# Kernel optimization log

Hardware: AMD Instinct MI355X
Metric: run time of the kernel (lower is better)

Reference implementation:

```python
import jax, jax.numpy as jnp
import numpy as np

BATCH = 8192
EMBED_DIM = 256
INPUT_DIM = 3 * EMBED_DIM  # 768
NUM_LAYERS = 4
VOCAB_SIZES = [100000, 100000, 1000]
EPS = 1e-5


def setup_inputs() -> dict:
    key = jax.random.key(0)
    ks = jax.random.split(key, 20)
    inp = {}
    inp["x_p"] = jax.random.randint(ks[0], (BATCH,), 0, VOCAB_SIZES[0])
    inp["x_a"] = jax.random.randint(ks[1], (BATCH,), 0, VOCAB_SIZES[1])
    inp["x_c"] = jax.random.randint(ks[2], (BATCH,), 0, VOCAB_SIZES[2])
    inp["y_true"] = jax.random.uniform(ks[3], (BATCH, 1), dtype=jnp.float32)
    # embedding tables (nn.Embedding default init N(0,1))
    inp["E0"] = jax.random.normal(ks[4], (VOCAB_SIZES[0], EMBED_DIM), dtype=jnp.float32)
    inp["E1"] = jax.random.normal(ks[5], (VOCAB_SIZES[1], EMBED_DIM), dtype=jnp.float32)
    inp["E2"] = jax.random.normal(ks[6], (VOCAB_SIZES[2], EMBED_DIM), dtype=jnp.float32)
    lim = 1.0 / np.sqrt(INPUT_DIM)
    inp["Wd"] = jax.random.uniform(ks[7], (NUM_LAYERS, INPUT_DIM, INPUT_DIM), jnp.float32, -lim, lim)
    inp["bd"] = jnp.zeros((NUM_LAYERS, INPUT_DIM), jnp.float32)
    inp["Ws"] = jax.random.uniform(ks[8], (NUM_LAYERS, INPUT_DIM, INPUT_DIM), jnp.float32, -lim, lim)
    inp["bs"] = jnp.zeros((NUM_LAYERS, INPUT_DIM), jnp.float32)
    inp["wfd"] = jax.random.uniform(ks[9], (INPUT_DIM,), jnp.float32, -lim, lim)
    inp["bfd"] = jax.random.uniform(ks[10], (), jnp.float32, -lim, lim)
    inp["wfs"] = jax.random.uniform(ks[11], (INPUT_DIM,), jnp.float32, -lim, lim)
    inp["bfs"] = jax.random.uniform(ks[12], (), jnp.float32, -lim, lim)
    return inp


def _cross_network(x, W, b, net_id, mask_key):
    # per layer: cross = x @ W[l].T + b[l]; mask = bernoulli(sigmoid(layernorm over FULL tensor)); x += cross*mask
    for l in range(NUM_LAYERS):
        cross = jnp.einsum("bd,od->bo", x, W[l]) + b[l]
        m = jnp.mean(cross)
        v = jnp.mean(jnp.square(cross - m))  # F.layer_norm(x, x.size()): normalize over all elements
        ln = (cross - m) * jax.lax.rsqrt(v + EPS)
        p = jax.nn.sigmoid(ln)
        k = jax.random.fold_in(mask_key, net_id * NUM_LAYERS + l)
        mask = jax.random.bernoulli(k, p).astype(x.dtype)
        x = x + cross * mask
    return x


def _bce(p, y):
    return jnp.mean(-(y * jnp.log(p) + (1.0 - y) * jnp.log(1.0 - p)))


def reference(x_p, x_a, x_c, y_true, E0, E1, E2, Wd, bd, Ws, bs, wfd, bfd, wfs, bfs):
    h = EMBED_DIM // 2
    e0, e1, e2 = E0[x_p], E1[x_a], E2[x_c]  # [B, embed_dim] each
    e_a = jnp.concatenate([e0[:, :h], e1[:, :h], e2[:, :h]], axis=-1)
    e_b = jnp.concatenate([e0[:, h:], e1[:, h:], e2[:, h:]], axis=-1)
    x = jnp.concatenate([e_a, e_b], axis=-1)  # [B, 3*embed_dim]

    mask_key = jax.random.key(42)
    x_d = _cross_network(x, Wd, bd, 0, mask_key)
    x_s = _cross_network(x, Ws, bs, 1, mask_key)

    sd_d = jax.nn.sigmoid(x_d @ wfd + bfd)[:, None]  # fc_d(x_d)
    ss_s = jax.nn.sigmoid(x_s @ wfs + bfs)[:, None]  # fc_s(x_s)
    sd_s = jax.nn.sigmoid(x_s @ wfd + bfd)[:, None]  # fc_d(x_s)
    ss_d = jax.nn.sigmoid(x_d @ wfs + bfs)[:, None]  # fc_s(x_d)
    y_pred_d = 0.5 * (sd_d + ss_s)
    y_pred_s = 0.5 * (sd_s + ss_d)

    loss_d = _bce(y_pred_d, y_true)
    loss_s = _bce(y_pred_s, y_true)
    bce_loss = loss_d + loss_s
    weight_d = jnp.maximum(0.0, loss_d - bce_loss)
    weight_s = jnp.maximum(0.0, loss_s - bce_loss)
    tri_loss = bce_loss + weight_d * loss_d + weight_s * loss_s
    return (y_pred_d, tri_loss)
```

## Files before the change

### kernel.cpp

```cpp
#include <hip/hip_runtime.h>
#include <hip/hip_bf16.h>
#include <cstdint>
#include <cstddef>

#define BATCH   8192
#define DIM     768
#define NTOT    6291456
#define NLAYERS 4

typedef _Float16 half8 __attribute__((ext_vector_type(8)));
typedef float    f32x4 __attribute__((ext_vector_type(4)));

#define AS_GLOBAL __attribute__((address_space(1)))
#define AS_LDS    __attribute__((address_space(3)))

__device__ __forceinline__ void async_copy16(const void* g, void* l) {
  __builtin_amdgcn_global_load_lds((AS_GLOBAL const uint32_t*)g,
                                   (AS_LDS uint32_t*)l, 16, 0, 0);
}

__host__ __device__ __forceinline__ uint32_t rotl32(uint32_t v, int d) {
  return (v << d) | (v >> (32 - d));
}

__host__ __device__ __forceinline__ void threefry2x32(
    uint32_t k0, uint32_t k1, uint32_t x0, uint32_t x1,
    uint32_t& o0, uint32_t& o1) {
  uint32_t ks2 = k0 ^ k1 ^ 0x1BD11BDAu;
  x0 += k0; x1 += k1;
#define TF_R(r) { x0 += x1; x1 = rotl32(x1, (r)) ^ x0; }
  TF_R(13) TF_R(15) TF_R(26) TF_R(6)
  x0 += k1; x1 += ks2 + 1u;
  TF_R(17) TF_R(29) TF_R(16) TF_R(24)
  x0 += ks2; x1 += k0 + 2u;
  TF_R(13) TF_R(15) TF_R(26) TF_R(6)
  x0 += k0; x1 += k1 + 3u;
  TF_R(17) TF_R(29) TF_R(16) TF_R(24)
  x0 += k1; x1 += ks2 + 4u;
  TF_R(13) TF_R(15) TF_R(26) TF_R(6)
  x0 += ks2; x1 += k0 + 5u;
#undef TF_R
  o0 = x0; o1 = x1;
}

__device__ __forceinline__ double sigmoid_d(double x) {
  return 1.0 / (1.0 + exp(-x));
}

__global__ __launch_bounds__(256) void gather_kernel(
    const int* __restrict__ x_p, const int* __restrict__ x_a,
    const int* __restrict__ x_c,
    const float* __restrict__ E0, const float* __restrict__ E1,
    const float* __restrict__ E2,
    _Float16* __restrict__ xdh, _Float16* __restrict__ xdl,
    _Float16* __restrict__ xsh, _Float16* __restrict__ xsl) {
  int j = blockIdx.x * 256 + threadIdx.x;
  int b = j / DIM;
  int f = j - b * DIM;
  int half_ = f / 384;
  int w = f - half_ * 384;
  int t = w >> 7;
  int c = (w & 127) + (half_ << 7);
  int idx;
  const float* E;
  if (t == 0)      { E = E0; idx = x_p[b]; }
  else if (t == 1) { E = E1; idx = x_a[b]; }
  else             { E = E2; idx = x_c[b]; }
  float v = E[(size_t)idx * 256 + c];
  _Float16 h = (_Float16)v;
  _Float16 l = (_Float16)(v - (float)h);
  xdh[j] = h; xdl[j] = l;
  xsh[j] = h; xsl[j] = l;
}

__global__ __launch_bounds__(256) void split_w_kernel(
    const float* __restrict__ Wd, const float* __restrict__ Ws,
    _Float16* __restrict__ Wh, _Float16* __restrict__ Wl) {
  int idx = blockIdx.x * 256 + threadIdx.x;
  const int perNet = NLAYERS * DIM * DIM;
  float v = (idx < perNet) ? Wd[idx] : Ws[idx - perNet];
  _Float16 h = (_Float16)v;
  Wh[idx] = h;
  Wl[idx] = (_Float16)(v - (float)h);
}

__global__ __launch_bounds__(256, 3) void gemm_mfma_kernel(
    const _Float16* __restrict__ xdh, const _Float16* __restrict__ xdl,
    const _Float16* __restrict__ xsh, const _Float16* __restrict__ xsl,
    const _Float16* __restrict__ Wh, const _Float16* __restrict__ Wl,
    const float* __restrict__ bd, const float* __restrict__ bs,
    float* __restrict__ crd, float* __restrict__ crs,
    double* __restrict__ partials, int layer) {
  const int net = blockIdx.z;
  const float* bias = (net ? bs : bd) + layer * DIM;
  float* C = net ? crs : crd;

  const int wave = threadIdx.x >> 6, lane = threadIdx.x & 63;
  const int quad = lane >> 4, l16 = lane & 15;
  const int m0 = blockIdx.x * 128;
  const int n0 = blockIdx.y * 128;

  __shared__ _Float16 lds[4 * 5120];

  const _Float16* gbase;
  int rowbase;
  switch (wave) {
    case 0:  gbase = net ? xsh : xdh; rowbase = m0; break;
    case 1:  gbase = net ? xsl : xdl; rowbase = m0; break;
    case 2:  gbase = Wh + ((size_t)net * NLAYERS + layer) * DIM * DIM; rowbase = n0; break;
    default: gbase = Wl + ((size_t)net * NLAYERS + layer) * DIM * DIM; rowbase = n0; break;
  }
  int soff[10];
#pragma unroll
  for (int j = 0; j < 10; ++j) {
    int s  = j * 64 + lane;
    int r  = (s * 52429) >> 18;
    int kk = (s - 5 * r) & 3;
    soff[j] = (rowbase + r) * DIM + kk * 8;
  }
  _Float16* ldsw = &lds[wave * 5120];

  const int wm = (wave >> 1) * 64, wn = (wave & 1) * 64;
  const int fslotA = ((wm + l16) * 5 + quad) * 8;
  const int fslotB = ((wn + l16) * 5 + quad) * 8;

  f32x4 acc[4][4];
#pragma unroll
  for (int i = 0; i < 4; ++i)
#pragma unroll
    for (int j = 0; j < 4; ++j) acc[i][j] = (f32x4){0.f, 0.f, 0.f, 0.f};

  for (int k0 = 0; k0 < DIM; k0 += 32) {
    __syncthreads();
#pragma unroll
    for (int j = 0; j < 10; ++j)
      async_copy16(gbase + soff[j] + k0, ldsw + j * 512);
    __syncthreads();

    half8 ah[4], al[4], bh[4], bl[4];
#pragma unroll
    for (int t = 0; t < 4; ++t) {
      ah[t] = *(const half8*)&lds[        fslotA + t * 640];
      al[t] = *(const half8*)&lds[ 5120 + fslotA + t * 640];
      bh[t] = *(const half8*)&lds[10240 + fslotB + t * 640];
      bl[t] = *(const half8*)&lds[15360 + fslotB + t * 640];
    }
#pragma unroll
    for (int mt = 0; mt < 4; ++mt)
#pragma unroll
      for (int nt = 0; nt < 4; ++nt) {
        f32x4 a = acc[mt][nt];
        a = __builtin_amdgcn_mfma_f32_16x16x32_f16(ah[mt], bh[nt], a, 0, 0, 0);
        a = __builtin_amdgcn_mfma_f32_16x16x32_f16(al[mt], bh[nt], a, 0, 0, 0);
        a = __builtin_amdgcn_mfma_f32_16x16x32_f16(ah[mt], bl[nt], a, 0, 0, 0);
        acc[mt][nt] = a;
      }
  }

  float biasv[4];
#pragma unroll
  for (int nt = 0; nt < 4; ++nt) biasv[nt] = bias[n0 + wn + nt * 16 + l16];

  double s = 0.0, q = 0.0;
#pragma unroll
  for (int mt = 0; mt < 4; ++mt) {
#pragma unroll
    for (int nt = 0; nt < 4; ++nt) {
      int n = n0 + wn + nt * 16 + l16;
#pragma unroll
      for (int r = 0; r < 4; ++r) {
        int m = m0 + wm + mt * 16 + quad * 4 + r;
        float v = acc[mt][nt][r] + biasv[nt];
        C[(size_t)m * DIM + n] = v;
        s += (double)v;
        q += (double)v * (double)v;
      }
    }
  }
#pragma unroll
  for (int off = 32; off > 0; off >>= 1) {
    s += __shfl_down(s, off);
    q += __shfl_down(q, off);
  }
  __shared__ double red[4][2];
  if (lane == 0) { red[wave][0] = s; red[wave][1] = q; }
  __syncthreads();
  if (threadIdx.x == 0) {
    double S = red[0][0] + red[1][0] + red[2][0] + red[3][0];
    double Q = red[0][1] + red[1][1] + red[2][1] + red[3][1];
    int bid = blockIdx.y * 64 + blockIdx.x;
    partials[((size_t)net * 384 + bid) * 2 + 0] = S;
    partials[((size_t)net * 384 + bid) * 2 + 1] = Q;
  }
}

__global__ __launch_bounds__(256) void finalize_stats_kernel(
    const double* __restrict__ partials, double* __restrict__ stats) {
  int net = blockIdx.x;
  const double* P = partials + (size_t)net * 384 * 2;
  int tid = threadIdx.x;
  double s = 0.0, q = 0.0;
  for (int i = tid; i < 384; i += 256) {
    s += P[i * 2 + 0];
    q += P[i * 2 + 1];
  }
#pragma unroll
  for (int off = 32; off > 0; off >>= 1) {
    s += __shfl_down(s, off);
    q += __shfl_down(q, off);
  }
  __shared__ double red[4][2];
  int wave = tid >> 6, lane = tid & 63;
  if (lane == 0) { red[wave][0] = s; red[wave][1] = q; }
  __syncthreads();
  if (tid == 0) {
    stats[net * 2 + 0] = red[0][0] + red[1][0] + red[2][0] + red[3][0];
    stats[net * 2 + 1] = red[0][1] + red[1][1] + red[2][1] + red[3][1];
  }
}

__global__ __launch_bounds__(256) void mask_update_kernel(
    _Float16* __restrict__ xdh, _Float16* __restrict__ xdl,
    _Float16* __restrict__ xsh, _Float16* __restrict__ xsl,
    const float* __restrict__ crd, const float* __restrict__ crs,
    const double* __restrict__ stats,
    uint32_t kd0, uint32_t kd1, uint32_t ks0, uint32_t ks1) {
  const int net = blockIdx.y;
  _Float16* xh = net ? xsh : xdh;
  _Float16* xl = net ? xsl : xdl;
  const float* cr = net ? crs : crd;
  const uint32_t k0 = net ? ks0 : kd0;
  const uint32_t k1 = net ? ks1 : kd1;

  const double invN = 1.0 / (double)NTOT;
  double meand = stats[net * 2 + 0] * invN;
  double vard  = stats[net * 2 + 1] * invN - meand * meand;
  float m  = (float)meand;
  float v  = (float)vard;
  float sv = v + 1e-5f;
  float rs = (float)(1.0 / sqrt((double)sv));

  uint32_t j = blockIdx.x * 256u + threadIdx.x;
  float c = cr[j];
  float ln = (c - m) * rs;
  float p = (float)sigmoid_d((double)ln);
  uint32_t o0, o1;
  threefry2x32(k0, k1, 0u, j, o0, o1);
  uint32_t bits = o0 ^ o1;
  float u = __uint_as_float(0x3F800000u | (bits >> 9)) - 1.0f;

  float xv = (float)xh[j] + (float)xl[j];
  if (u < p) xv += c;
  _Float16 h = (_Float16)xv;
  xh[j] = h;
  xl[j] = (_Float16)(xv - (float)h);
}

__global__ __launch_bounds__(256) void head_kernel(
    const _Float16* __restrict__ xdh, const _Float16* __restrict__ xdl,
    const _Float16* __restrict__ xsh, const _Float16* __restrict__ xsl,
    const float* __restrict__ wfd, const float* __restrict__ wfs,
    const float* __restrict__ bfd_p, const float* __restrict__ bfs_p,
    const float* __restrict__ y_true,
    float* __restrict__ out, double* __restrict__ bce_part) {
  const int wave = threadIdx.x >> 6;
  const int lane = threadIdx.x & 63;
  const int row = blockIdx.x * 4 + wave;
  const size_t base = (size_t)row * DIM;

  float dd = 0.f, dsw = 0.f, sd = 0.f, ssw = 0.f;
  for (int t = lane; t < DIM; t += 64) {
    float vd = (float)xdh[base + t] + (float)xdl[base + t];
    float vs = (float)xsh[base + t] + (float)xsl[base + t];
    float wd = wfd[t], ws = wfs[t];
    dd  = fmaf(vd, wd, dd);
    dsw = fmaf(vd, ws, dsw);
    sd  = fmaf(vs, wd, sd);
    ssw = fmaf(vs, ws, ssw);
  }
#pragma unroll
  for (int off = 32; off > 0; off >>= 1) {
    dd  += __shfl_down(dd, off);
    dsw += __shfl_down(dsw, off);
    sd  += __shfl_down(sd, off);
    ssw += __shfl_down(ssw, off);
  }
  __shared__ double redd[4], reds[4];
  if (lane == 0) {
    float bfd = *bfd_p, bfs = *bfs_p;
    double sdd = sigmoid_d((double)(dd + bfd));
    double ssd = sigmoid_d((double)(dsw + bfs));
    double sds = sigmoid_d((double)(sd + bfd));
    double sss = sigmoid_d((double)(ssw + bfs));
    double ypd = 0.5 * (sdd + sss);
    double yps = 0.5 * (sds + ssd);
    out[row] = (float)ypd;
    double y = (double)y_true[row];
    redd[wave] = -(y * log(ypd) + (1.0 - y) * log(1.0 - ypd));
    reds[wave] = -(y * log(yps) + (1.0 - y) * log(1.0 - yps));
  }
  __syncthreads();
  if (threadIdx.x == 0) {
    bce_part[(size_t)blockIdx.x * 2 + 0] = redd[0] + redd[1] + redd[2] + redd[3];
    bce_part[(size_t)blockIdx.x * 2 + 1] = reds[0] + reds[1] + reds[2] + reds[3];
  }
}

__global__ __launch_bounds__(256) void loss_kernel(
    const double* __restrict__ bce_part, float* __restrict__ out_tri) {
  int tid = threadIdx.x;
  double sdl = 0.0, ssl = 0.0;
  for (int i = tid; i < 2048; i += 256) {
    sdl += bce_part[i * 2 + 0];
    ssl += bce_part[i * 2 + 1];
  }
#pragma unroll
  for (int off = 32; off > 0; off >>= 1) {
    sdl += __shfl_down(sdl, off);
    ssl += __shfl_down(ssl, off);
  }
  __shared__ double red[4][2];
  int wave = tid >> 6, lane = tid & 63;
  if (lane == 0) { red[wave][0] = sdl; red[wave][1] = ssl; }
  __syncthreads();
  if (tid == 0) {
    double loss_d = (red[0][0] + red[1][0] + red[2][0] + red[3][0]) / (double)BATCH;
    double loss_s = (red[0][1] + red[1][1] + red[2][1] + red[3][1]) / (double)BATCH;
    double bce = loss_d + loss_s;
    double wd = fmax(0.0, loss_d - bce);
    double ws = fmax(0.0, loss_s - bce);
    out_tri[0] = (float)(bce + wd * loss_d + ws * loss_s);
  }
}

extern "C" void kernel_launch(void* const* d_in, const int* in_sizes, int n_in,
                              void* d_out, int out_size, void* d_ws, size_t ws_size,
                              hipStream_t stream) {
  const int* x_p = (const int*)d_in[0];
  const int* x_a = (const int*)d_in[1];
  const int* x_c = (const int*)d_in[2];
  const float* y_true = (const float*)d_in[3];
  const float* E0 = (const float*)d_in[4];
  const float* E1 = (const float*)d_in[5];
  const float* E2 = (const float*)d_in[6];
  const float* Wd = (const float*)d_in[7];
  const float* bd = (const float*)d_in[8];
  const float* Ws = (const float*)d_in[9];
  const float* bs = (const float*)d_in[10];
  const float* wfd = (const float*)d_in[11];
  const float* bfd = (const float*)d_in[12];
  const float* wfs = (const float*)d_in[13];
  const float* bfs = (const float*)d_in[14];
  float* out = (float*)d_out;

  char* p = (char*)d_ws;
  float* crd = (float*)p;                 p += (size_t)NTOT * 4;
  float* crs = (float*)p;                 p += (size_t)NTOT * 4;
  double* partials = (double*)p;          p += (size_t)2 * 384 * 2 * 8;
  double* stats    = (double*)p;          p += 4 * 8;
  double* bce_part = (double*)p;          p += (size_t)2048 * 2 * 8;
  _Float16* xdh = (_Float16*)p;           p += (size_t)NTOT * 2;
  _Float16* xdl = (_Float16*)p;           p += (size_t)NTOT * 2;
  _Float16* xsh = (_Float16*)p;           p += (size_t)NTOT * 2;
  _Float16* xsl = (_Float16*)p;           p += (size_t)NTOT * 2;
  _Float16* Wh  = (_Float16*)p;           p += (size_t)2 * NLAYERS * DIM * DIM * 2;
  _Float16* Wl  = (_Float16*)p;           p += (size_t)2 * NLAYERS * DIM * DIM * 2;

  gather_kernel<<<NTOT / 256, 256, 0, stream>>>(
      x_p, x_a, x_c, E0, E1, E2, xdh, xdl, xsh, xsl);
  split_w_kernel<<<2 * NLAYERS * DIM * DIM / 256, 256, 0, stream>>>(Wd, Ws, Wh, Wl);

  for (int l = 0; l < NLAYERS; ++l) {
    gemm_mfma_kernel<<<dim3(64, 6, 2), 256, 0, stream>>>(
        xdh, xdl, xsh, xsl, Wh, Wl, bd, bs, crd, crs, partials, l);
    finalize_stats_kernel<<<2, 256, 0, stream>>>(partials, stats);
    uint32_t kd0, kd1, ks0, ks1;
    threefry2x32(0u, 42u, 0u, (uint32_t)l, kd0, kd1);
    threefry2x32(0u, 42u, 0u, (uint32_t)(4 + l), ks0, ks1);
    mask_update_kernel<<<dim3(NTOT / 256, 2), 256, 0, stream>>>(
        xdh, xdl, xsh, xsl, crd, crs, stats, kd0, kd1, ks0, ks1);
  }

  head_kernel<<<BATCH / 4, 256, 0, stream>>>(
      xdh, xdl, xsh, xsl, wfd, wfs, bfd, bfs, y_true, out, bce_part);
  loss_kernel<<<1, 256, 0, stream>>>(bce_part, out + BATCH);
}
```

Baseline: 800.6 us.

## Retile GEMM with double-buffered LDS, atomic stats, and vectorized elementwise kernels

```diff
diff --git a/kernel.cpp b/kernel.cpp
--- a/kernel.cpp
+++ b/kernel.cpp
@@ -9,6 +9,7 @@
 #define NLAYERS 4
 
 typedef _Float16 half8 __attribute__((ext_vector_type(8)));
+typedef _Float16 half4 __attribute__((ext_vector_type(4)));
 typedef float    f32x4 __attribute__((ext_vector_type(4)));
 
 #define AS_GLOBAL __attribute__((address_space(1)))
@@ -47,30 +48,63 @@
   return 1.0 / (1.0 + exp(-x));
 }
 
+__device__ __forceinline__ double dexp(double x) {
+  x = fmin(fmax(x, -708.0), 708.0);
+  const double LOG2E = 1.4426950408889634;
+  const double LN2   = 0.6931471805599453;
+  double t = x * LOG2E;
+  double n = rint(t);
+  double g = (t - n) * LN2;
+  double r = 2.7557319223985893e-07;
+  r = r * g + 2.7557319223985888e-06;
+  r = r * g + 2.4801587301587302e-05;
+  r = r * g + 1.9841269841269841e-04;
+  r = r * g + 1.3888888888888889e-03;
+  r = r * g + 8.3333333333333332e-03;
+  r = r * g + 4.1666666666666664e-02;
+  r = r * g + 1.6666666666666666e-01;
+  r = r * g + 0.5;
+  r = r * g + 1.0;
+  r = r * g + 1.0;
+  int ni = (int)n;
+  double sc = __longlong_as_double(((long long)(1023 + ni)) << 52);
+  return r * sc;
+}
+
 __global__ __launch_bounds__(256) void gather_kernel(
     const int* __restrict__ x_p, const int* __restrict__ x_a,
     const int* __restrict__ x_c,
     const float* __restrict__ E0, const float* __restrict__ E1,
     const float* __restrict__ E2,
     _Float16* __restrict__ xdh, _Float16* __restrict__ xdl,
-    _Float16* __restrict__ xsh, _Float16* __restrict__ xsl) {
-  int j = blockIdx.x * 256 + threadIdx.x;
-  int b = j / DIM;
-  int f = j - b * DIM;
+    _Float16* __restrict__ xsh, _Float16* __restrict__ xsl,
+    double* __restrict__ stats, double* __restrict__ bce_acc) {
+  if (blockIdx.x == 0 && threadIdx.x < 18) {
+    if (threadIdx.x < 16) stats[threadIdx.x] = 0.0;
+    else bce_acc[threadIdx.x - 16] = 0.0;
+  }
+  int j4  = blockIdx.x * 256 + threadIdx.x;
+  int idx = j4 * 4;
+  int b = idx / DIM;
+  int f = idx - b * DIM;
   int half_ = f / 384;
   int w = f - half_ * 384;
   int t = w >> 7;
   int c = (w & 127) + (half_ << 7);
-  int idx;
+  int row;
   const float* E;
-  if (t == 0)      { E = E0; idx = x_p[b]; }
-  else if (t == 1) { E = E1; idx = x_a[b]; }
-  else             { E = E2; idx = x_c[b]; }
-  float v = E[(size_t)idx * 256 + c];
-  _Float16 h = (_Float16)v;
-  _Float16 l = (_Float16)(v - (float)h);
-  xdh[j] = h; xdl[j] = l;
-  xsh[j] = h; xsl[j] = l;
+  if (t == 0)      { E = E0; row = x_p[b]; }
+  else if (t == 1) { E = E1; row = x_a[b]; }
+  else             { E = E2; row = x_c[b]; }
+  f32x4 v = *(const f32x4*)&E[(size_t)row * 256 + c];
+  half4 h, l;
+#pragma unroll
+  for (int i = 0; i < 4; ++i) {
+    h[i] = (_Float16)v[i];
+    l[i] = (_Float16)(v[i] - (float)h[i]);
+  }
+  *(half4*)&xdh[idx] = h; *(half4*)&xdl[idx] = l;
+  *(half4*)&xsh[idx] = h; *(half4*)&xsl[idx] = l;
 }
 
 __global__ __launch_bounds__(256) void split_w_kernel(
@@ -84,138 +118,127 @@
   Wl[idx] = (_Float16)(v - (float)h);
 }
 
-__global__ __launch_bounds__(256, 3) void gemm_mfma_kernel(
+__global__ __launch_bounds__(512, 2) void gemm_mfma_kernel(
     const _Float16* __restrict__ xdh, const _Float16* __restrict__ xdl,
     const _Float16* __restrict__ xsh, const _Float16* __restrict__ xsl,
     const _Float16* __restrict__ Wh, const _Float16* __restrict__ Wl,
     const float* __restrict__ bd, const float* __restrict__ bs,
     float* __restrict__ crd, float* __restrict__ crs,
-    double* __restrict__ partials, int layer) {
+    double* __restrict__ stats, int layer) {
   const int net = blockIdx.z;
   const float* bias = (net ? bs : bd) + layer * DIM;
   float* C = net ? crs : crd;
 
-  const int wave = threadIdx.x >> 6, lane = threadIdx.x & 63;
+  const int tid  = threadIdx.x;
+  const int wave = tid >> 6, lane = tid & 63;
   const int quad = lane >> 4, l16 = lane & 15;
   const int m0 = blockIdx.x * 128;
-  const int n0 = blockIdx.y * 128;
-
-  __shared__ _Float16 lds[4 * 5120];
+  const int n0 = blockIdx.y * 384;
+
+  __shared__ _Float16 lds[2][32768];
+  __shared__ double red[8][2];
 
   const _Float16* gbase;
-  int rowbase;
-  switch (wave) {
-    case 0:  gbase = net ? xsh : xdh; rowbase = m0; break;
-    case 1:  gbase = net ? xsl : xdl; rowbase = m0; break;
-    case 2:  gbase = Wh + ((size_t)net * NLAYERS + layer) * DIM * DIM; rowbase = n0; break;
-    default: gbase = Wl + ((size_t)net * NLAYERS + layer) * DIM * DIM; rowbase = n0; break;
-  }
-  int soff[10];
-#pragma unroll
-  for (int j = 0; j < 10; ++j) {
-    int s  = j * 64 + lane;
-    int r  = (s * 52429) >> 18;
-    int kk = (s - 5 * r) & 3;
+  int chunkoff, rows, rowbase;
+  if (wave == 0)      { gbase = net ? xsh : xdh; chunkoff = 0; rows = 128; rowbase = m0; }
+  else if (wave == 1) { gbase = net ? xsl : xdl; chunkoff = 0; rows = 128; rowbase = m0; }
+  else if (wave < 5)  { gbase = Wh + ((size_t)net * NLAYERS + layer) * DIM * DIM;
+                        chunkoff = (wave - 2) * 512; rows = 384; rowbase = n0; }
+  else                { gbase = Wl + ((size_t)net * NLAYERS + layer) * DIM * DIM;
+                        chunkoff = (wave - 5) * 512; rows = 384; rowbase = n0; }
+  int soff[8];
+#pragma unroll
+  for (int j = 0; j < 8; ++j) {
+    int s  = chunkoff + j * 64 + lane;
+    int kk = s / rows;
+    int r  = s - kk * rows;
     soff[j] = (rowbase + r) * DIM + kk * 8;
   }
-  _Float16* ldsw = &lds[wave * 5120];
-
-  const int wm = (wave >> 1) * 64, wn = (wave & 1) * 64;
-  const int fslotA = ((wm + l16) * 5 + quad) * 8;
-  const int fslotB = ((wn + l16) * 5 + quad) * 8;
-
-  f32x4 acc[4][4];
+  const int ldsbase = wave * 4096;
+
+  const int wm = (wave >> 2) * 64;
+  const int wn = (wave & 3) * 96;
+
+  f32x4 acc[4][6];
 #pragma unroll
   for (int i = 0; i < 4; ++i)
 #pragma unroll
-    for (int j = 0; j < 4; ++j) acc[i][j] = (f32x4){0.f, 0.f, 0.f, 0.f};
-
-  for (int k0 = 0; k0 < DIM; k0 += 32) {
-    __syncthreads();
-#pragma unroll
-    for (int j = 0; j < 10; ++j)
-      async_copy16(gbase + soff[j] + k0, ldsw + j * 512);
-    __syncthreads();
-
-    half8 ah[4], al[4], bh[4], bl[4];
-#pragma unroll
-    for (int t = 0; t < 4; ++t) {
-      ah[t] = *(const half8*)&lds[        fslotA + t * 640];
-      al[t] = *(const half8*)&lds[ 5120 + fslotA + t * 640];
-      bh[t] = *(const half8*)&lds[10240 + fslotB + t * 640];
-      bl[t] = *(const half8*)&lds[15360 + fslotB + t * 640];
+    for (int j = 0; j < 6; ++j) acc[i][j] = (f32x4){0.f, 0.f, 0.f, 0.f};
+
+#pragma unroll
+  for (int j = 0; j < 8; ++j)
+    async_copy16(gbase + soff[j], &lds[0][ldsbase + j * 512]);
+  __syncthreads();
+
+  int cur = 0;
+  for (int s = 0; s < 24; ++s) {
+    if (s < 23) {
+      const int k0n = (s + 1) * 32;
+#pragma unroll
+      for (int j = 0; j < 8; ++j)
+        async_copy16(gbase + soff[j] + k0n, &lds[cur ^ 1][ldsbase + j * 512]);
     }
-#pragma unroll
-    for (int mt = 0; mt < 4; ++mt)
-#pragma unroll
-      for (int nt = 0; nt < 4; ++nt) {
+    half8 ah[4], al[4];
+#pragma unroll
+    for (int mt = 0; mt < 4; ++mt) {
+      int g = quad * 128 + wm + mt * 16 + l16;
+      ah[mt] = *(const half8*)&lds[cur][g * 8];
+      al[mt] = *(const half8*)&lds[cur][4096 + g * 8];
+    }
+    __builtin_amdgcn_s_setprio(1);
+#pragma unroll
+    for (int nt = 0; nt < 6; ++nt) {
+      int g = quad * 384 + wn + nt * 16 + l16;
+      half8 bh = *(const half8*)&lds[cur][8192  + g * 8];
+      half8 bl = *(const half8*)&lds[cur][20480 + g * 8];
+#pragma unroll
+      for (int mt = 0; mt < 4; ++mt) {
         f32x4 a = acc[mt][nt];
-        a = __builtin_amdgcn_mfma_f32_16x16x32_f16(ah[mt], bh[nt], a, 0, 0, 0);
-        a = __builtin_amdgcn_mfma_f32_16x16x32_f16(al[mt], bh[nt], a, 0, 0, 0);
-        a = __builtin_amdgcn_mfma_f32_16x16x32_f16(ah[mt], bl[nt], a, 0, 0, 0);
+        a = __builtin_amdgcn_mfma_f32_16x16x32_f16(ah[mt], bh, a, 0, 0, 0);
+        a = __builtin_amdgcn_mfma_f32_16x16x32_f16(al[mt], bh, a, 0, 0, 0);
+        a = __builtin_amdgcn_mfma_f32_16x16x32_f16(ah[mt], bl, a, 0, 0, 0);
         acc[mt][nt] = a;
       }
-  }
-
-  float biasv[4];
-#pragma unroll
-  for (int nt = 0; nt < 4; ++nt) biasv[nt] = bias[n0 + wn + nt * 16 + l16];
-
-  double s = 0.0, q = 0.0;
+    }
+    __builtin_amdgcn_s_setprio(0);
+    __syncthreads();
+    cur ^= 1;
+  }
+
+  float biasv[6];
+#pragma unroll
+  for (int nt = 0; nt < 6; ++nt) biasv[nt] = bias[n0 + wn + nt * 16 + l16];
+
+  double S = 0.0, Q = 0.0;
 #pragma unroll
   for (int mt = 0; mt < 4; ++mt) {
 #pragma unroll
-    for (int nt = 0; nt < 4; ++nt) {
+    for (int nt = 0; nt < 6; ++nt) {
       int n = n0 + wn + nt * 16 + l16;
 #pragma unroll
       for (int r = 0; r < 4; ++r) {
         int m = m0 + wm + mt * 16 + quad * 4 + r;
         float v = acc[mt][nt][r] + biasv[nt];
         C[(size_t)m * DIM + n] = v;
-        s += (double)v;
-        q += (double)v * (double)v;
+        S += (double)v;
+        Q += (double)v * (double)v;
       }
     }
   }
 #pragma unroll
   for (int off = 32; off > 0; off >>= 1) {
-    s += __shfl_down(s, off);
-    q += __shfl_down(q, off);
-  }
-  __shared__ double red[4][2];
-  if (lane == 0) { red[wave][0] = s; red[wave][1] = q; }
-  __syncthreads();
-  if (threadIdx.x == 0) {
-    double S = red[0][0] + red[1][0] + red[2][0] + red[3][0];
-    double Q = red[0][1] + red[1][1] + red[2][1] + red[3][1];
-    int bid = blockIdx.y * 64 + blockIdx.x;
-    partials[((size_t)net * 384 + bid) * 2 + 0] = S;
-    partials[((size_t)net * 384 + bid) * 2 + 1] = Q;
-  }
-}
-
-__global__ __launch_bounds__(256) void finalize_stats_kernel(
-    const double* __restrict__ partials, double* __restrict__ stats) {
-  int net = blockIdx.x;
-  const double* P = partials + (size_t)net * 384 * 2;
-  int tid = threadIdx.x;
-  double s = 0.0, q = 0.0;
-  for (int i = tid; i < 384; i += 256) {
-    s += P[i * 2 + 0];
-    q += P[i * 2 + 1];
-  }
-#pragma unroll
-  for (int off = 32; off > 0; off >>= 1) {
-    s += __shfl_down(s, off);
-    q += __shfl_down(q, off);
-  }
-  __shared__ double red[4][2];
-  int wave = tid >> 6, lane = tid & 63;
-  if (lane == 0) { red[wave][0] = s; red[wave][1] = q; }
+    S += __shfl_down(S, off);
+    Q += __shfl_down(Q, off);
+  }
+  if (lane == 0) { red[wave][0] = S; red[wave][1] = Q; }
   __syncthreads();
   if (tid == 0) {
-    stats[net * 2 + 0] = red[0][0] + red[1][0] + red[2][0] + red[3][0];
-    stats[net * 2 + 1] = red[0][1] + red[1][1] + red[2][1] + red[3][1];
+    double s2 = 0.0, q2 = 0.0;
+#pragma unroll
+    for (int wv = 0; wv < 8; ++wv) { s2 += red[wv][0]; q2 += red[wv][1]; }
+    double* st = stats + ((size_t)layer * 2 + net) * 2;
+    atomicAdd(&st[0], s2);
+    atomicAdd(&st[1], q2);
   }
 }
 
@@ -223,7 +246,7 @@
     _Float16* __restrict__ xdh, _Float16* __restrict__ xdl,
     _Float16* __restrict__ xsh, _Float16* __restrict__ xsl,
     const float* __restrict__ crd, const float* __restrict__ crs,
-    const double* __restrict__ stats,
+    const double* __restrict__ stats, int layer,
     uint32_t kd0, uint32_t kd1, uint32_t ks0, uint32_t ks1) {
   const int net = blockIdx.y;
   _Float16* xh = net ? xsh : xdh;
@@ -233,27 +256,39 @@
   const uint32_t k1 = net ? ks1 : kd1;
 
   const double invN = 1.0 / (double)NTOT;
-  double meand = stats[net * 2 + 0] * invN;
-  double vard  = stats[net * 2 + 1] * invN - meand * meand;
+  const double* st = stats + ((size_t)layer * 2 + net) * 2;
+  double meand = st[0] * invN;
+  double vard  = st[1] * invN - meand * meand;
   float m  = (float)meand;
   float v  = (float)vard;
   float sv = v + 1e-5f;
   float rs = (float)(1.0 / sqrt((double)sv));
 
-  uint32_t j = blockIdx.x * 256u + threadIdx.x;
-  float c = cr[j];
-  float ln = (c - m) * rs;
-  float p = (float)sigmoid_d((double)ln);
-  uint32_t o0, o1;
-  threefry2x32(k0, k1, 0u, j, o0, o1);
-  uint32_t bits = o0 ^ o1;
-  float u = __uint_as_float(0x3F800000u | (bits >> 9)) - 1.0f;
-
-  float xv = (float)xh[j] + (float)xl[j];
-  if (u < p) xv += c;
-  _Float16 h = (_Float16)xv;
-  xh[j] = h;
-  xl[j] = (_Float16)(xv - (float)h);
+  uint32_t j0 = (blockIdx.x * 256u + threadIdx.x) * 8u;
+  float cc[8];
+  *(f32x4*)&cc[0] = *(const f32x4*)&cr[j0];
+  *(f32x4*)&cc[4] = *(const f32x4*)&cr[j0 + 4];
+  half8 h8 = *(const half8*)&xh[j0];
+  half8 l8 = *(const half8*)&xl[j0];
+  half8 ho, lo;
+#pragma unroll
+  for (int i = 0; i < 8; ++i) {
+    float c  = cc[i];
+    float ln = (c - m) * rs;
+    uint32_t o0, o1;
+    threefry2x32(k0, k1, 0u, j0 + (uint32_t)i, o0, o1);
+    uint32_t bits = o0 ^ o1;
+    float u = __uint_as_float(0x3F800000u | (bits >> 9)) - 1.0f;
+    double e  = dexp(-(double)ln);
+    double ue = (double)u;
+    float xv = (float)h8[i] + (float)l8[i];
+    if (ue + ue * e < 1.0) xv += c;
+    _Float16 hh = (_Float16)xv;
+    ho[i] = hh;
+    lo[i] = (_Float16)(xv - (float)hh);
+  }
+  *(half8*)&xh[j0] = ho;
+  *(half8*)&xl[j0] = lo;
 }
 
 __global__ __launch_bounds__(256) void head_kernel(
@@ -262,21 +297,28 @@
     const float* __restrict__ wfd, const float* __restrict__ wfs,
     const float* __restrict__ bfd_p, const float* __restrict__ bfs_p,
     const float* __restrict__ y_true,
-    float* __restrict__ out, double* __restrict__ bce_part) {
+    float* __restrict__ out, double* __restrict__ bce_acc) {
   const int wave = threadIdx.x >> 6;
   const int lane = threadIdx.x & 63;
   const int row = blockIdx.x * 4 + wave;
   const size_t base = (size_t)row * DIM;
 
   float dd = 0.f, dsw = 0.f, sd = 0.f, ssw = 0.f;
-  for (int t = lane; t < DIM; t += 64) {
-    float vd = (float)xdh[base + t] + (float)xdl[base + t];
-    float vs = (float)xsh[base + t] + (float)xsl[base + t];
-    float wd = wfd[t], ws = wfs[t];
-    dd  = fmaf(vd, wd, dd);
-    dsw = fmaf(vd, ws, dsw);
-    sd  = fmaf(vs, wd, sd);
-    ssw = fmaf(vs, ws, ssw);
+  for (int cb = lane; cb < 96; cb += 64) {
+    half8 hd = *(const half8*)&xdh[base + cb * 8];
+    half8 ld = *(const half8*)&xdl[base + cb * 8];
+    half8 hs = *(const half8*)&xsh[base + cb * 8];
+    half8 ls = *(const half8*)&xsl[base + cb * 8];
+#pragma unroll
+    for (int i = 0; i < 8; ++i) {
+      float vd = (float)hd[i] + (float)ld[i];
+      float vs = (float)hs[i] + (float)ls[i];
+      float wd = wfd[cb * 8 + i], ws = wfs[cb * 8 + i];
+      dd  = fmaf(vd, wd, dd);
+      dsw = fmaf(vd, ws, dsw);
+      sd  = fmaf(vs, wd, sd);
+      ssw = fmaf(vs, ws, ssw);
+    }
   }
 #pragma unroll
   for (int off = 32; off > 0; off >>= 1) {
@@ -301,31 +343,16 @@
   }
   __syncthreads();
   if (threadIdx.x == 0) {
-    bce_part[(size_t)blockIdx.x * 2 + 0] = redd[0] + redd[1] + redd[2] + redd[3];
-    bce_part[(size_t)blockIdx.x * 2 + 1] = reds[0] + reds[1] + reds[2] + reds[3];
-  }
-}
-
-__global__ __launch_bounds__(256) void loss_kernel(
-    const double* __restrict__ bce_part, float* __restrict__ out_tri) {
-  int tid = threadIdx.x;
-  double sdl = 0.0, ssl = 0.0;
-  for (int i = tid; i < 2048; i += 256) {
-    sdl += bce_part[i * 2 + 0];
-    ssl += bce_part[i * 2 + 1];
-  }
-#pragma unroll
-  for (int off = 32; off > 0; off >>= 1) {
-    sdl += __shfl_down(sdl, off);
-    ssl += __shfl_down(ssl, off);
-  }
-  __shared__ double red[4][2];
-  int wave = tid >> 6, lane = tid & 63;
-  if (lane == 0) { red[wave][0] = sdl; red[wave][1] = ssl; }
-  __syncthreads();
-  if (tid == 0) {
-    double loss_d = (red[0][0] + red[1][0] + red[2][0] + red[3][0]) / (double)BATCH;
-    double loss_s = (red[0][1] + red[1][1] + red[2][1] + red[3][1]) / (double)BATCH;
+    atomicAdd(&bce_acc[0], redd[0] + redd[1] + redd[2] + redd[3]);
+    atomicAdd(&bce_acc[1], reds[0] + reds[1] + reds[2] + reds[3]);
+  }
+}
+
+__global__ void loss_kernel(const double* __restrict__ bce_acc,
+                            float* __restrict__ out_tri) {
+  if (threadIdx.x == 0) {
+    double loss_d = bce_acc[0] / (double)BATCH;
+    double loss_s = bce_acc[1] / (double)BATCH;
     double bce = loss_d + loss_s;
     double wd = fmax(0.0, loss_d - bce);
     double ws = fmax(0.0, loss_s - bce);
@@ -356,9 +383,8 @@
   char* p = (char*)d_ws;
   float* crd = (float*)p;                 p += (size_t)NTOT * 4;
   float* crs = (float*)p;                 p += (size_t)NTOT * 4;
-  double* partials = (double*)p;          p += (size_t)2 * 384 * 2 * 8;
-  double* stats    = (double*)p;          p += 4 * 8;
-  double* bce_part = (double*)p;          p += (size_t)2048 * 2 * 8;
+  double* stats   = (double*)p;           p += (size_t)16 * 8;
+  double* bce_acc = (double*)p;           p += (size_t)2 * 8;
   _Float16* xdh = (_Float16*)p;           p += (size_t)NTOT * 2;
   _Float16* xdl = (_Float16*)p;           p += (size_t)NTOT * 2;
   _Float16* xsh = (_Float16*)p;           p += (size_t)NTOT * 2;
@@ -366,22 +392,21 @@
   _Float16* Wh  = (_Float16*)p;           p += (size_t)2 * NLAYERS * DIM * DIM * 2;
   _Float16* Wl  = (_Float16*)p;           p += (size_t)2 * NLAYERS * DIM * DIM * 2;
 
-  gather_kernel<<<NTOT / 256, 256, 0, stream>>>(
-      x_p, x_a, x_c, E0, E1, E2, xdh, xdl, xsh, xsl);
+  gather_kernel<<<NTOT / 1024, 256, 0, stream>>>(
+      x_p, x_a, x_c, E0, E1, E2, xdh, xdl, xsh, xsl, stats, bce_acc);
   split_w_kernel<<<2 * NLAYERS * DIM * DIM / 256, 256, 0, stream>>>(Wd, Ws, Wh, Wl);
 
   for (int l = 0; l < NLAYERS; ++l) {
-    gemm_mfma_kernel<<<dim3(64, 6, 2), 256, 0, stream>>>(
-        xdh, xdl, xsh, xsl, Wh, Wl, bd, bs, crd, crs, partials, l);
-    finalize_stats_kernel<<<2, 256, 0, stream>>>(partials, stats);
+    gemm_mfma_kernel<<<dim3(64, 2, 2), 512, 0, stream>>>(
+        xdh, xdl, xsh, xsl, Wh, Wl, bd, bs, crd, crs, stats, l);
     uint32_t kd0, kd1, ks0, ks1;
     threefry2x32(0u, 42u, 0u, (uint32_t)l, kd0, kd1);
     threefry2x32(0u, 42u, 0u, (uint32_t)(4 + l), ks0, ks1);
-    mask_update_kernel<<<dim3(NTOT / 256, 2), 256, 0, stream>>>(
-        xdh, xdl, xsh, xsl, crd, crs, stats, kd0, kd1, ks0, ks1);
+    mask_update_kernel<<<dim3(NTOT / 2048, 2), 256, 0, stream>>>(
+        xdh, xdl, xsh, xsl, crd, crs, stats, l, kd0, kd1, ks0, ks1);
   }
 
   head_kernel<<<BATCH / 4, 256, 0, stream>>>(
-      xdh, xdl, xsh, xsl, wfd, wfs, bfd, bfs, y_true, out, bce_part);
-  loss_kernel<<<1, 256, 0, stream>>>(bce_part, out + BATCH);
-}
+      xdh, xdl, xsh, xsl, wfd, wfs, bfd, bfs, y_true, out, bce_acc);
+  loss_kernel<<<1, 64, 0, stream>>>(bce_acc, out + BATCH);
+}
```

After: 903.1 us. 1.13x slower.
